# Performance work log

Hardware: AMD Instinct MI355X
Metric: run time of the kernel (lower is better)

Reference implementation:

```python
import jax, jax.numpy as jnp
import numpy as np

B = 1048576
N_BINS = 128


def setup_inputs() -> dict:
    key = jax.random.key(0)
    k1, k2 = jax.random.split(key)
    # input: probabilities-ish in [0,1], shape [B, n_bins]
    inp = jax.random.uniform(k1, (B, N_BINS), dtype=jnp.float32)
    # bins: sorted bin edge values (sorted for realism; math doesn't require it)
    bins = jnp.sort(jax.random.normal(k2, (N_BINS,), dtype=jnp.float32))
    return {"input": inp, "bins": bins}


def reference(input, bins):
    # scores[:,0]=0; scores[:,i+1]=scores[:,i]+1-2*input[:,i]  == exclusive-prefixed cumsum
    deltas = 1.0 - 2.0 * input                      # [B, n]
    zeros = jnp.zeros((input.shape[0], 1), dtype=input.dtype)
    scores = jnp.concatenate([zeros, jnp.cumsum(deltas, axis=1)], axis=1)  # [B, n+1]
    indices = jnp.argmin(scores, axis=1)            # [B]
    bins_to_select = jnp.concatenate([bins[:1], bins, bins[-1:]])          # [n+2]
    chosen = (bins_to_select[indices] + bins_to_select[indices + 1]) * 0.5 # [B]
    return chosen[:, None]
```

## Files before the change

### kernel.cpp

```cpp
#include <hip/hip_runtime.h>


#define NBINS  128
#define ROWS   128
#define CHUNK  32
#define NCHUNK (NBINS / CHUNK)

__global__ __launch_bounds__(ROWS) void fitstep_kernel(
    const float* __restrict__ inp,
    const float* __restrict__ bins,
    float* __restrict__ out,
    int nrows)
{
    __shared__ float lds[2][ROWS * CHUNK];

    const int t = threadIdx.x;
    const size_t rowbase = (size_t)blockIdx.x * ROWS;

    if (rowbase + ROWS <= (size_t)nrows) {
        const char* base = (const char*)(inp + rowbase * NBINS);

        const int r0   = t >> 3;
        const int jswz = (t & 7) ^ (r0 & 7);
        const size_t goff0 = (size_t)r0 * (NBINS * 4) + (size_t)jswz * 16;

        auto stage = [&](int c, int buf) {
            const char* gc = base + goff0 + (size_t)c * (CHUNK * 4);
            #pragma unroll
            for (int i = 0; i < 8; ++i) {
                __builtin_amdgcn_global_load_lds(
                    (const __attribute__((address_space(1))) unsigned int*)
                        (gc + (size_t)i * 16 * (NBINS * 4)),
                    (__attribute__((address_space(3))) unsigned int*)
                        (&lds[buf][(i * ROWS + t) * 4]),
                    16, 0, 0);
            }
        };

        stage(0, 0);
        __syncthreads();

        float score = 0.0f, best = 0.0f;
        int bestIdx = 0;

        for (int c = 0; c < NCHUNK; ++c) {
            const int buf = c & 1;

            if (c + 1 < NCHUNK) stage(c + 1, buf ^ 1);

            #pragma unroll
            for (int j = 0; j < 8; ++j) {
                const int slot = j ^ (t & 7);
                float4 v = *reinterpret_cast<const float4*>(
                    &lds[buf][t * CHUNK + slot * 4]);
                int colbase = c * CHUNK + j * 4;
                score += (1.0f - 2.0f * v.x);
                if (score < best) { best = score; bestIdx = colbase + 1; }
                score += (1.0f - 2.0f * v.y);
                if (score < best) { best = score; bestIdx = colbase + 2; }
                score += (1.0f - 2.0f * v.z);
                if (score < best) { best = score; bestIdx = colbase + 3; }
                score += (1.0f - 2.0f * v.w);
                if (score < best) { best = score; bestIdx = colbase + 4; }
            }

            if (c + 1 < NCHUNK) __syncthreads();
        }

        int lo = bestIdx - 1; if (lo < 0) lo = 0;
        int hi = bestIdx;     if (hi > NBINS - 1) hi = NBINS - 1;
        out[rowbase + t] = (bins[lo] + bins[hi]) * 0.5f;
    } else {
        size_t row = rowbase + t;
        if (row >= (size_t)nrows) return;
        const float* rp = inp + row * NBINS;
        float score = 0.0f, best = 0.0f;
        int bestIdx = 0;
        for (int j = 0; j < NBINS; ++j) {
            score += (1.0f - 2.0f * rp[j]);
            if (score < best) { best = score; bestIdx = j + 1; }
        }
        int lo = bestIdx - 1; if (lo < 0) lo = 0;
        int hi = bestIdx;     if (hi > NBINS - 1) hi = NBINS - 1;
        out[row] = (bins[lo] + bins[hi]) * 0.5f;
    }
}

extern "C" void kernel_launch(void* const* d_in, const int* in_sizes, int n_in,
                              void* d_out, int out_size, void* d_ws, size_t ws_size,
                              hipStream_t stream)
{
    const float* inp  = (const float*)d_in[0];
    const float* bins = (const float*)d_in[1];
    float* out = (float*)d_out;

    int nrows = in_sizes[0] / NBINS;
    int grid  = (nrows + ROWS - 1) / ROWS;

    fitstep_kernel<<<grid, ROWS, 0, stream>>>(inp, bins, out, nrows);
}
```

Measured before the change: 98.18 us.

## Use single-wave blocks and issue all chunk loads upfront with vmcnt waits

Blocks shrink from 128 to 64 rows, so each block is a single wavefront. That wavefront issues all four chunks' global-to-LDS loads at once into four separate LDS buffers. Before each chunk is scanned, it waits with explicit s_waitcnt vmcnt counts instead of double buffering with __syncthreads. The aim is to remove the barriers and keep more loads in flight per wave. In exchange, LDS per thread doubles, which halves the number of resident waves per CU, and correctness now depends on the hand-set vmcnt values and on each block being exactly one wave.

```diff
diff --git a/kernel.cpp b/kernel.cpp
--- a/kernel.cpp
+++ b/kernel.cpp
@@ -2,7 +2,7 @@
 
 
 #define NBINS  128
-#define ROWS   128
+#define ROWS   64
 #define CHUNK  32
 #define NCHUNK (NBINS / CHUNK)
 
@@ -12,7 +12,7 @@
     float* __restrict__ out,
     int nrows)
 {
-    __shared__ float lds[2][ROWS * CHUNK];
+    __shared__ float lds[NCHUNK][ROWS * CHUNK];
 
     const int t = threadIdx.x;
     const size_t rowbase = (size_t)blockIdx.x * ROWS;
@@ -20,39 +20,34 @@
     if (rowbase + ROWS <= (size_t)nrows) {
         const char* base = (const char*)(inp + rowbase * NBINS);
 
-        const int r0   = t >> 3;
-        const int jswz = (t & 7) ^ (r0 & 7);
-        const size_t goff0 = (size_t)r0 * (NBINS * 4) + (size_t)jswz * 16;
+        const int    jswz     = (t & 7) ^ ((t >> 3) & 7);
+        const size_t lanebase = (size_t)(t >> 3) * (NBINS * 4) + (size_t)jswz * 16;
 
-        auto stage = [&](int c, int buf) {
-            const char* gc = base + goff0 + (size_t)c * (CHUNK * 4);
+        #pragma unroll
+        for (int c = 0; c < NCHUNK; ++c) {
             #pragma unroll
             for (int i = 0; i < 8; ++i) {
                 __builtin_amdgcn_global_load_lds(
                     (const __attribute__((address_space(1))) unsigned int*)
-                        (gc + (size_t)i * 16 * (NBINS * 4)),
+                        (base + lanebase
+                              + (size_t)i * 8 * (NBINS * 4)
+                              + (size_t)c * (CHUNK * 4)),
                     (__attribute__((address_space(3))) unsigned int*)
-                        (&lds[buf][(i * ROWS + t) * 4]),
+                        (&lds[c][(i * ROWS + t) * 4]),
                     16, 0, 0);
             }
-        };
-
-        stage(0, 0);
-        __syncthreads();
+            asm volatile("" ::: "memory");
+        }
 
         float score = 0.0f, best = 0.0f;
         int bestIdx = 0;
 
-        for (int c = 0; c < NCHUNK; ++c) {
-            const int buf = c & 1;
-
-            if (c + 1 < NCHUNK) stage(c + 1, buf ^ 1);
-
+        auto scan_chunk = [&](int c) {
             #pragma unroll
             for (int j = 0; j < 8; ++j) {
                 const int slot = j ^ (t & 7);
                 float4 v = *reinterpret_cast<const float4*>(
-                    &lds[buf][t * CHUNK + slot * 4]);
+                    &lds[c][t * CHUNK + slot * 4]);
                 int colbase = c * CHUNK + j * 4;
                 score += (1.0f - 2.0f * v.x);
                 if (score < best) { best = score; bestIdx = colbase + 1; }
@@ -63,9 +58,16 @@
                 score += (1.0f - 2.0f * v.w);
                 if (score < best) { best = score; bestIdx = colbase + 4; }
             }
+        };
 
-            if (c + 1 < NCHUNK) __syncthreads();
-        }
+        asm volatile("s_waitcnt vmcnt(24)" ::: "memory");
+        scan_chunk(0);
+        asm volatile("s_waitcnt vmcnt(16)" ::: "memory");
+        scan_chunk(1);
+        asm volatile("s_waitcnt vmcnt(8)" ::: "memory");
+        scan_chunk(2);
+        asm volatile("s_waitcnt vmcnt(0)" ::: "memory");
+        scan_chunk(3);
 
         int lo = bestIdx - 1; if (lo < 0) lo = 0;
         int hi = bestIdx;     if (hi > NBINS - 1) hi = NBINS - 1;
```

Result: no change. 98.10 us (-0.1%).

## Replace async global-to-LDS loads with register-staged double buffering, 256-row blocks

Applied to the files above, without the earlier changes.

Drops the direct global_load_lds staging and instead loads each chunk into registers (two register sets) before writing it to swizzled LDS. This keeps two chunks of global loads in flight ahead of the scan, with a fully unrolled four-chunk schedule. Block size doubles to 256 rows and launch bounds request 4 blocks per CU. The cost is more VGPRs (64 floats of staging per thread) and 64KB of LDS per block, which may limit occupancy.

```diff
diff --git a/kernel.cpp b/kernel.cpp
--- a/kernel.cpp
+++ b/kernel.cpp
@@ -2,11 +2,11 @@
 
 
 #define NBINS  128
-#define ROWS   128
+#define ROWS   256
 #define CHUNK  32
 #define NCHUNK (NBINS / CHUNK)
 
-__global__ __launch_bounds__(ROWS) void fitstep_kernel(
+__global__ __launch_bounds__(ROWS, 4) void fitstep_kernel(
     const float* __restrict__ inp,
     const float* __restrict__ bins,
     float* __restrict__ out,
@@ -18,36 +18,33 @@
     const size_t rowbase = (size_t)blockIdx.x * ROWS;
 
     if (rowbase + ROWS <= (size_t)nrows) {
-        const char* base = (const char*)(inp + rowbase * NBINS);
+        const float* base = inp + rowbase * NBINS;
 
-        const int r0   = t >> 3;
-        const int jswz = (t & 7) ^ (r0 & 7);
-        const size_t goff0 = (size_t)r0 * (NBINS * 4) + (size_t)jswz * 16;
+        float4 RA[8], RB[8];
 
-        auto stage = [&](int c, int buf) {
-            const char* gc = base + goff0 + (size_t)c * (CHUNK * 4);
+        auto gload = [&](int c, float4 (&R)[8]) {
             #pragma unroll
             for (int i = 0; i < 8; ++i) {
-                __builtin_amdgcn_global_load_lds(
-                    (const __attribute__((address_space(1))) unsigned int*)
-                        (gc + (size_t)i * 16 * (NBINS * 4)),
-                    (__attribute__((address_space(3))) unsigned int*)
-                        (&lds[buf][(i * ROWS + t) * 4]),
-                    16, 0, 0);
+                int f = i * ROWS + t;
+                int r = f >> 3, k = f & 7;
+                R[i] = *reinterpret_cast<const float4*>(
+                    base + (size_t)r * NBINS + c * CHUNK + k * 4);
             }
         };
-
-        stage(0, 0);
-        __syncthreads();
+        auto stage = [&](float4 (&R)[8], int buf) {
+            #pragma unroll
+            for (int i = 0; i < 8; ++i) {
+                int f = i * ROWS + t;
+                int r = f >> 3, k = f & 7;
+                int slot = k ^ (r & 7);
+                *reinterpret_cast<float4*>(&lds[buf][r * CHUNK + slot * 4]) = R[i];
+            }
+        };
 
         float score = 0.0f, best = 0.0f;
         int bestIdx = 0;
 
-        for (int c = 0; c < NCHUNK; ++c) {
-            const int buf = c & 1;
-
-            if (c + 1 < NCHUNK) stage(c + 1, buf ^ 1);
-
+        auto scan_chunk = [&](int c, int buf) {
             #pragma unroll
             for (int j = 0; j < 8; ++j) {
                 const int slot = j ^ (t & 7);
@@ -63,9 +60,25 @@
                 score += (1.0f - 2.0f * v.w);
                 if (score < best) { best = score; bestIdx = colbase + 4; }
             }
+        };
 
-            if (c + 1 < NCHUNK) __syncthreads();
-        }
+        gload(0, RA);
+        gload(1, RB);
+        stage(RA, 0);
+        __syncthreads();
+
+        gload(2, RA);
+        scan_chunk(0, 0);
+        stage(RB, 1);
+        __syncthreads();
+        gload(3, RB);
+        scan_chunk(1, 1);
+        stage(RA, 0);
+        __syncthreads();
+        scan_chunk(2, 0);
+        stage(RB, 1);
+        __syncthreads();
+        scan_chunk(3, 1);
 
         int lo = bestIdx - 1; if (lo < 0) lo = 0;
         int hi = bestIdx;     if (hi > NBINS - 1) hi = NBINS - 1;
```

After: 216.5 us. 121% more time.

## Replace block-synchronized LDS DMA double buffer with per-wave register-prefetch pipeline

Applied to the files above, without the earlier changes.

Each 64-lane wave now owns its own 64-row LDS tile in a 256-thread block. Chunks are prefetched from global memory into registers as float4 loads and then written swizzled into LDS after the current chunk is scanned. The direct global-to-LDS loads and the block-wide __syncthreads are gone, so each wave pipelines on its own schedule and does not stall on the other waves. In exchange it uses more VGPRs for the prefetch registers, adds explicit LDS store instructions, and relies on in-wave ordering to reuse a single LDS buffer.

```diff
diff --git a/kernel.cpp b/kernel.cpp
--- a/kernel.cpp
+++ b/kernel.cpp
@@ -2,57 +2,59 @@
 
 
 #define NBINS  128
-#define ROWS   128
 #define CHUNK  32
 #define NCHUNK (NBINS / CHUNK)
+#define BLOCK  256
+#define WROWS  64
 
-__global__ __launch_bounds__(ROWS) void fitstep_kernel(
+__global__ __launch_bounds__(BLOCK) void fitstep_kernel(
     const float* __restrict__ inp,
     const float* __restrict__ bins,
     float* __restrict__ out,
     int nrows)
 {
-    __shared__ float lds[2][ROWS * CHUNK];
+    __shared__ float lds[BLOCK / 64][WROWS * CHUNK];
 
     const int t = threadIdx.x;
-    const size_t rowbase = (size_t)blockIdx.x * ROWS;
+    const int w = t >> 6;
+    const int l = t & 63;
+    const size_t rowbase = (size_t)blockIdx.x * BLOCK + (size_t)w * WROWS;
 
-    if (rowbase + ROWS <= (size_t)nrows) {
-        const char* base = (const char*)(inp + rowbase * NBINS);
+    if (rowbase + WROWS <= (size_t)nrows) {
+        const float* gbase = inp + rowbase * NBINS;
+        float* myLds = lds[w];
 
-        const int r0   = t >> 3;
-        const int jswz = (t & 7) ^ (r0 & 7);
-        const size_t goff0 = (size_t)r0 * (NBINS * 4) + (size_t)jswz * 16;
+        const int r0  = l >> 3;
+        const int k   = l & 7;
+        const int swz = k ^ r0;
 
-        auto stage = [&](int c, int buf) {
-            const char* gc = base + goff0 + (size_t)c * (CHUNK * 4);
+        float4 R[8];
+
+        auto gload = [&](int c) {
             #pragma unroll
             for (int i = 0; i < 8; ++i) {
-                __builtin_amdgcn_global_load_lds(
-                    (const __attribute__((address_space(1))) unsigned int*)
-                        (gc + (size_t)i * 16 * (NBINS * 4)),
-                    (__attribute__((address_space(3))) unsigned int*)
-                        (&lds[buf][(i * ROWS + t) * 4]),
-                    16, 0, 0);
+                int r = 8 * i + r0;
+                R[i] = *reinterpret_cast<const float4*>(
+                    gbase + (size_t)r * NBINS + c * CHUNK + k * 4);
             }
         };
-
-        stage(0, 0);
-        __syncthreads();
+        auto stage = [&]() {
+            #pragma unroll
+            for (int i = 0; i < 8; ++i) {
+                int r = 8 * i + r0;
+                *reinterpret_cast<float4*>(&myLds[r * CHUNK + swz * 4]) = R[i];
+            }
+        };
 
         float score = 0.0f, best = 0.0f;
         int bestIdx = 0;
 
-        for (int c = 0; c < NCHUNK; ++c) {
-            const int buf = c & 1;
-
-            if (c + 1 < NCHUNK) stage(c + 1, buf ^ 1);
-
+        auto scan_chunk = [&](int c) {
             #pragma unroll
             for (int j = 0; j < 8; ++j) {
-                const int slot = j ^ (t & 7);
+                const int slot = j ^ k;
                 float4 v = *reinterpret_cast<const float4*>(
-                    &lds[buf][t * CHUNK + slot * 4]);
+                    &myLds[l * CHUNK + slot * 4]);
                 int colbase = c * CHUNK + j * 4;
                 score += (1.0f - 2.0f * v.x);
                 if (score < best) { best = score; bestIdx = colbase + 1; }
@@ -63,15 +65,23 @@
                 score += (1.0f - 2.0f * v.w);
                 if (score < best) { best = score; bestIdx = colbase + 4; }
             }
+        };
 
-            if (c + 1 < NCHUNK) __syncthreads();
+        gload(0);
+        stage();
+
+        #pragma unroll
+        for (int c = 0; c < NCHUNK; ++c) {
+            if (c + 1 < NCHUNK) gload(c + 1);
+            scan_chunk(c);
+            if (c + 1 < NCHUNK) stage();
         }
 
         int lo = bestIdx - 1; if (lo < 0) lo = 0;
         int hi = bestIdx;     if (hi > NBINS - 1) hi = NBINS - 1;
-        out[rowbase + t] = (bins[lo] + bins[hi]) * 0.5f;
+        out[rowbase + l] = (bins[lo] + bins[hi]) * 0.5f;
     } else {
-        size_t row = rowbase + t;
+        size_t row = rowbase + l;
         if (row >= (size_t)nrows) return;
         const float* rp = inp + row * NBINS;
         float score = 0.0f, best = 0.0f;
@@ -95,7 +105,7 @@
     float* out = (float*)d_out;
 
     int nrows = in_sizes[0] / NBINS;
-    int grid  = (nrows + ROWS - 1) / ROWS;
+    int grid  = (nrows + BLOCK - 1) / BLOCK;
 
-    fitstep_kernel<<<grid, ROWS, 0, stream>>>(inp, bins, out, nrows);
+    fitstep_kernel<<<grid, BLOCK, 0, stream>>>(inp, bins, out, nrows);
 }
```

Result: slower. 177.0 us (+80.3%).
